# Kernel tuning notes

Hardware: AMD Instinct MI355X
Metric: run time of the kernel (lower is better)

Reference implementation:

```python
import jax, jax.numpy as jnp
import numpy as np

B, CIN, COUT, L = 16, 128, 128, 4096  # kernel_size == L required by the broadcast in the source
STRIDE, DIL, PAD = 1, 1, 0


def setup_inputs() -> dict:
    key = jax.random.key(0)
    kx, kw, kb = jax.random.split(key, 3)
    x = jax.random.normal(kx, (B, CIN, L), dtype=jnp.float32)
    # source does weight.data.int() then .float() in forward -> integer-truncated randn
    weight = jnp.trunc(jax.random.normal(kw, (COUT, CIN, L), dtype=jnp.float32))
    bias = jax.random.normal(kb, (COUT,), dtype=jnp.float32)
    return {"x": x, "weight": weight, "bias": bias}


def reference(x, weight, bias):
    # padding=0 -> F.pad is a no-op; output_size = (L + 2*0 - 1*(K-1) - 1)//1 + 1 = 1
    out_size = (L + 2 * PAD - DIL * (L - 1) - 1) // STRIDE + 1  # == 1
    x_f = jnp.fft.fft(x, axis=2)            # [B, Cin, L] complex64
    w_f = jnp.fft.fft(weight, axis=2)       # [Cout, Cin, L] complex64
    # faithful math of (x_f[:,None] * w_f[None]).sum(dim=2), expressed as a
    # per-frequency complex contraction to avoid the O(B*Cout*Cin*L) intermediate
    out_f = jnp.einsum('bil,oil->bol', x_f, w_f)  # [B, Cout, L]
    out = jnp.fft.ifft(out_f, axis=2).real
    out = out + bias[None, :, None]
    return out[:, :, :out_size]
```

## Files before the change

kernel.cpp:

```cpp
#include <hip/hip_runtime.h>


constexpr int LEN   = 4096;
constexpr int CIN_  = 128;
constexpr int COUT_ = 128;
constexpr int BATCH = 16;

__global__ void init_out_kernel(const float* __restrict__ bias, float* __restrict__ out) {
    int t = blockIdx.x * 256 + threadIdx.x;
    if (t < BATCH * COUT_) out[t] = bias[t & (COUT_ - 1)];
}

__device__ __forceinline__ void gload_lds4(const float* g, float* l) {
    __builtin_amdgcn_global_load_lds(
        (const __attribute__((address_space(1))) unsigned int*)g,
        (__attribute__((address_space(3))) unsigned int*)l, 4, 0, 0);
}

__device__ __forceinline__ void stage_chunk(const float* __restrict__ x, float* dst_base,
                                            int ci, int m0, int wv, int lane) {
#pragma unroll
    for (int bb = 0; bb < 2; ++bb) {
        const int b = 2 * wv + bb;
        const float* xc = x + ((b * CIN_ + ci) << 12);
        float* dstb = dst_base + (b << 9);
#pragma unroll
        for (int t = 0; t < 8; ++t) {
            const int n = (LEN - m0 - (t << 6) - lane) & (LEN - 1);
            gload_lds4(xc + n, dstb + (t << 6));
        }
    }
}

__global__ __launch_bounds__(512, 2)
void conv_fft_dot_kernel(const float* __restrict__ x, const float* __restrict__ w,
                         float* __restrict__ out) {
    __shared__ float lds[17408];

    const int tid   = threadIdx.x;
    const int lane  = tid & 63;
    const int wv    = __builtin_amdgcn_readfirstlane(tid >> 6);
    const int bk    = blockIdx.x;
    const int ot    = bk >> 7;
    const int ci    = bk & 127;
    const int obase = ot * 16 + wv * 2;

    const float* wr0 = w + (((obase + 0) * CIN_ + ci) << 12);
    const float* wr1 = w + (((obase + 1) * CIN_ + ci) << 12);

    float acc[16][2];
#pragma unroll
    for (int b = 0; b < 16; ++b) { acc[b][0] = 0.f; acc[b][1] = 0.f; }

    stage_chunk(x, lds, ci, 0, wv, lane);
    __builtin_amdgcn_sched_barrier(0);
    float4 wa0 = ((const float4*)wr0)[lane];
    float4 wa1 = ((const float4*)wr1)[lane];
    asm volatile("s_waitcnt vmcnt(2)" ::: "memory");
    __builtin_amdgcn_s_barrier();
    __builtin_amdgcn_sched_barrier(0);

#pragma unroll 1
    for (int q = 0; q < 8; ++q) {
        const int m0 = q << 9;
        const float4* __restrict__ xb = (const float4*)(lds + ((q & 1) << 13));

        float4 wb0 = ((const float4*)(wr0 + m0 + 256))[lane];
        float4 wb1 = ((const float4*)(wr1 + m0 + 256))[lane];

        if (q < 7)
            stage_chunk(x, lds + (((q + 1) & 1) << 13), ci, (q + 1) << 9, wv, lane);

#pragma unroll
        for (int b = 0; b < 16; ++b) {
            const float4 xv = xb[(b << 7) + lane];
            acc[b][0] += xv.x * wa0.x; acc[b][0] += xv.y * wa0.y;
            acc[b][0] += xv.z * wa0.z; acc[b][0] += xv.w * wa0.w;
            acc[b][1] += xv.x * wa1.x; acc[b][1] += xv.y * wa1.y;
            acc[b][1] += xv.z * wa1.z; acc[b][1] += xv.w * wa1.w;
        }

        __builtin_amdgcn_sched_barrier(0);

        if (q < 7) {
            wa0 = ((const float4*)(wr0 + m0 + 512))[lane];
            wa1 = ((const float4*)(wr1 + m0 + 512))[lane];
        }

#pragma unroll
        for (int b = 0; b < 16; ++b) {
            const float4 xv = xb[(b << 7) + 64 + lane];
            acc[b][0] += xv.x * wb0.x; acc[b][0] += xv.y * wb0.y;
            acc[b][0] += xv.z * wb0.z; acc[b][0] += xv.w * wb0.w;
            acc[b][1] += xv.x * wb1.x; acc[b][1] += xv.y * wb1.y;
            acc[b][1] += xv.z * wb1.z; acc[b][1] += xv.w * wb1.w;
        }

        if (q < 7) {
            asm volatile("s_waitcnt vmcnt(2)" ::: "memory");
            __builtin_amdgcn_s_barrier();
            __builtin_amdgcn_sched_barrier(0);
        }
    }

    __syncthreads();
#pragma unroll
    for (int b = 0; b < 16; ++b) {
        lds[(wv * 32 + b * 2 + 0) * 68 + lane] = acc[b][0];
        lds[(wv * 32 + b * 2 + 1) * 68 + lane] = acc[b][1];
    }
    __syncthreads();
    if (tid < 256) {
        const float4* row = (const float4*)(lds + tid * 68);
        float sum = 0.f;
#pragma unroll
        for (int l = 0; l < 16; ++l) {
            const float4 v = row[l];
            sum += v.x + v.y + v.z + v.w;
        }
        const int wv2 = tid >> 5, r = tid & 31;
        const int b = r >> 1, jj = r & 1;
        const int o = ot * 16 + wv2 * 2 + jj;
        atomicAdd(out + b * COUT_ + o, sum);
    }
}

extern "C" void kernel_launch(void* const* d_in, const int* in_sizes, int n_in,
                              void* d_out, int out_size, void* d_ws, size_t ws_size,
                              hipStream_t stream) {
    const float* x    = (const float*)d_in[0];
    const float* wgt  = (const float*)d_in[1];
    const float* bias = (const float*)d_in[2];
    float* out = (float*)d_out;
    (void)in_sizes; (void)n_in; (void)d_ws; (void)ws_size; (void)out_size;

    init_out_kernel<<<8, 256, 0, stream>>>(bias, out);
    conv_fft_dot_kernel<<<1024, 512, 0, stream>>>(x, wgt, out);
}
```

Baseline: 393.6 us.

## Widen per-wave output tile to four channels and deepen x staging pipeline

Each wave now computes four output channels instead of two, so every LDS-staged x value is reused twice as often and the grid shrinks to 512 blocks, halving the total number of x reloads. Staging switches to 256-element chunks in a four-deep LDS ring with two chunks in flight, and weights are read with nontemporal loads to avoid polluting cache. The cost is double the accumulator registers (64 floats), which may push occupancy down, plus a four-pass epilogue reduction with extra barriers.

```diff
diff --git a/kernel.cpp b/kernel.cpp
--- a/kernel.cpp
+++ b/kernel.cpp
@@ -6,9 +6,15 @@
 constexpr int COUT_ = 128;
 constexpr int BATCH = 16;
 
+typedef float f32x4 __attribute__((ext_vector_type(4)));
+
 __global__ void init_out_kernel(const float* __restrict__ bias, float* __restrict__ out) {
     int t = blockIdx.x * 256 + threadIdx.x;
     if (t < BATCH * COUT_) out[t] = bias[t & (COUT_ - 1)];
+}
+
+__device__ __forceinline__ f32x4 ntload4(const float* p) {
+    return __builtin_nontemporal_load((const f32x4*)p);
 }
 
 __device__ __forceinline__ void gload_lds4(const float* g, float* l) {
@@ -17,25 +23,22 @@
         (__attribute__((address_space(3))) unsigned int*)l, 4, 0, 0);
 }
 
-__device__ __forceinline__ void stage_chunk(const float* __restrict__ x, float* dst_base,
-                                            int ci, int m0, int wv, int lane) {
+__device__ __forceinline__ void stage256(const float* xc0, const float* xc1,
+                                         float* buf, int m0, int wv, int lane) {
+    float* d0 = buf + ((2 * wv + 0) << 8);
+    float* d1 = buf + ((2 * wv + 1) << 8);
 #pragma unroll
-    for (int bb = 0; bb < 2; ++bb) {
-        const int b = 2 * wv + bb;
-        const float* xc = x + ((b * CIN_ + ci) << 12);
-        float* dstb = dst_base + (b << 9);
-#pragma unroll
-        for (int t = 0; t < 8; ++t) {
-            const int n = (LEN - m0 - (t << 6) - lane) & (LEN - 1);
-            gload_lds4(xc + n, dstb + (t << 6));
-        }
+    for (int t = 0; t < 4; ++t) {
+        const int n = (LEN - m0 - (t << 6) - lane) & (LEN - 1);
+        gload_lds4(xc0 + n, d0 + (t << 6));
+        gload_lds4(xc1 + n, d1 + (t << 6));
     }
 }
 
 __global__ __launch_bounds__(512, 2)
 void conv_fft_dot_kernel(const float* __restrict__ x, const float* __restrict__ w,
                          float* __restrict__ out) {
-    __shared__ float lds[17408];
+    __shared__ float lds[16384];
 
     const int tid   = threadIdx.x;
     const int lane  = tid & 63;
@@ -43,85 +46,101 @@
     const int bk    = blockIdx.x;
     const int ot    = bk >> 7;
     const int ci    = bk & 127;
-    const int obase = ot * 16 + wv * 2;
+    const int obase = ot * 32 + wv * 4;
 
+    const float* xc0 = x + (((2 * wv + 0) * CIN_ + ci) << 12);
+    const float* xc1 = x + (((2 * wv + 1) * CIN_ + ci) << 12);
     const float* wr0 = w + (((obase + 0) * CIN_ + ci) << 12);
     const float* wr1 = w + (((obase + 1) * CIN_ + ci) << 12);
+    const float* wr2 = w + (((obase + 2) * CIN_ + ci) << 12);
+    const float* wr3 = w + (((obase + 3) * CIN_ + ci) << 12);
+    const int lo = lane << 2;
 
-    float acc[16][2];
+    float acc[16][4];
 #pragma unroll
-    for (int b = 0; b < 16; ++b) { acc[b][0] = 0.f; acc[b][1] = 0.f; }
+    for (int b = 0; b < 16; ++b)
+#pragma unroll
+        for (int j = 0; j < 4; ++j) acc[b][j] = 0.f;
 
-    stage_chunk(x, lds, ci, 0, wv, lane);
+    stage256(xc0, xc1, lds, 0, wv, lane);
     __builtin_amdgcn_sched_barrier(0);
-    float4 wa0 = ((const float4*)wr0)[lane];
-    float4 wa1 = ((const float4*)wr1)[lane];
-    asm volatile("s_waitcnt vmcnt(2)" ::: "memory");
+    stage256(xc0, xc1, lds + 4096, 256, wv, lane);
+    __builtin_amdgcn_sched_barrier(0);
+    f32x4 wc[4];
+    wc[0] = ntload4(wr0 + lo); wc[1] = ntload4(wr1 + lo);
+    wc[2] = ntload4(wr2 + lo); wc[3] = ntload4(wr3 + lo);
+    asm volatile("s_waitcnt vmcnt(12)" ::: "memory");
     __builtin_amdgcn_s_barrier();
     __builtin_amdgcn_sched_barrier(0);
 
 #pragma unroll 1
-    for (int q = 0; q < 8; ++q) {
-        const int m0 = q << 9;
-        const float4* __restrict__ xb = (const float4*)(lds + ((q & 1) << 13));
-
-        float4 wb0 = ((const float4*)(wr0 + m0 + 256))[lane];
-        float4 wb1 = ((const float4*)(wr1 + m0 + 256))[lane];
-
-        if (q < 7)
-            stage_chunk(x, lds + (((q + 1) & 1) << 13), ci, (q + 1) << 9, wv, lane);
-
-#pragma unroll
-        for (int b = 0; b < 16; ++b) {
-            const float4 xv = xb[(b << 7) + lane];
-            acc[b][0] += xv.x * wa0.x; acc[b][0] += xv.y * wa0.y;
-            acc[b][0] += xv.z * wa0.z; acc[b][0] += xv.w * wa0.w;
-            acc[b][1] += xv.x * wa1.x; acc[b][1] += xv.y * wa1.y;
-            acc[b][1] += xv.z * wa1.z; acc[b][1] += xv.w * wa1.w;
+    for (int qq = 0; qq < 16; qq += 4) {
+#define BODY(K)                                                               \
+        {                                                                     \
+            const int q  = qq + (K);                                          \
+            const int m0 = q << 8;                                            \
+            f32x4 wn[4];                                                      \
+            if (q < 15) {     \
+                wn[0] = ntload4(wr0 + m0 + 256 + lo);                         \
+                wn[1] = ntload4(wr1 + m0 + 256 + lo);                         \
+                wn[2] = ntload4(wr2 + m0 + 256 + lo);                         \
+                wn[3] = ntload4(wr3 + m0 + 256 + lo);                         \
+            }                                                                 \
+            if (q < 14)       \
+                stage256(xc0, xc1, lds + ((((K) + 2) & 3) << 12),             \
+                         m0 + 512, wv, lane);                                 \
+            __builtin_amdgcn_sched_barrier(0);                                \
+            const float4* xb = (const float4*)(lds + (((K) & 3) << 12));      \
+            _Pragma("unroll")                                                 \
+            for (int b = 0; b < 16; ++b) {                                    \
+                const float4 xv = xb[(b << 6) + lane];                        \
+                _Pragma("unroll")                                             \
+                for (int j = 0; j < 4; ++j) {                                 \
+                    acc[b][j] += xv.x * wc[j].x;                              \
+                    acc[b][j] += xv.y * wc[j].y;                              \
+                    acc[b][j] += xv.z * wc[j].z;                              \
+                    acc[b][j] += xv.w * wc[j].w;                              \
+                }                                                             \
+            }                                                                 \
+            __builtin_amdgcn_sched_barrier(0);                                \
+            if (q < 15) {                                                     \
+                wc[0] = wn[0]; wc[1] = wn[1]; wc[2] = wn[2]; wc[3] = wn[3];   \
+            }                                                                 \
+            if (q < 14)                                                       \
+                asm volatile("s_waitcnt vmcnt(12)" ::: "memory");             \
+            else if (q == 14)                                                 \
+                asm volatile("s_waitcnt vmcnt(4)" ::: "memory");              \
+            if (q < 15) {                                                     \
+                __builtin_amdgcn_s_barrier();                                 \
+                __builtin_amdgcn_sched_barrier(0);                            \
+            }                                                                 \
         }
-
-        __builtin_amdgcn_sched_barrier(0);
-
-        if (q < 7) {
-            wa0 = ((const float4*)(wr0 + m0 + 512))[lane];
-            wa1 = ((const float4*)(wr1 + m0 + 512))[lane];
-        }
-
-#pragma unroll
-        for (int b = 0; b < 16; ++b) {
-            const float4 xv = xb[(b << 7) + 64 + lane];
-            acc[b][0] += xv.x * wb0.x; acc[b][0] += xv.y * wb0.y;
-            acc[b][0] += xv.z * wb0.z; acc[b][0] += xv.w * wb0.w;
-            acc[b][1] += xv.x * wb1.x; acc[b][1] += xv.y * wb1.y;
-            acc[b][1] += xv.z * wb1.z; acc[b][1] += xv.w * wb1.w;
-        }
-
-        if (q < 7) {
-            asm volatile("s_waitcnt vmcnt(2)" ::: "memory");
-            __builtin_amdgcn_s_barrier();
-            __builtin_amdgcn_sched_barrier(0);
-        }
+        BODY(0) BODY(1) BODY(2) BODY(3)
+#undef BODY
     }
 
     __syncthreads();
 #pragma unroll
-    for (int b = 0; b < 16; ++b) {
-        lds[(wv * 32 + b * 2 + 0) * 68 + lane] = acc[b][0];
-        lds[(wv * 32 + b * 2 + 1) * 68 + lane] = acc[b][1];
-    }
-    __syncthreads();
-    if (tid < 256) {
-        const float4* row = (const float4*)(lds + tid * 68);
-        float sum = 0.f;
+    for (int p = 0; p < 4; ++p) {
+        if (p) __syncthreads();
 #pragma unroll
-        for (int l = 0; l < 16; ++l) {
-            const float4 v = row[l];
-            sum += v.x + v.y + v.z + v.w;
+        for (int bb = 0; bb < 4; ++bb)
+#pragma unroll
+            for (int j = 0; j < 4; ++j)
+                lds[(wv * 16 + bb * 4 + j) * 68 + lane] = acc[p * 4 + bb][j];
+        __syncthreads();
+        if (tid < 128) {
+            const float4* row = (const float4*)(lds + tid * 68);
+            float sum = 0.f;
+#pragma unroll
+            for (int l = 0; l < 16; ++l) {
+                const float4 v = row[l];
+                sum += v.x + v.y + v.z + v.w;
+            }
+            const int o = ot * 32 + (tid >> 4) * 4 + (tid & 3);
+            const int b = p * 4 + ((tid >> 2) & 3);
+            atomicAdd(out + b * COUT_ + o, sum);
         }
-        const int wv2 = tid >> 5, r = tid & 31;
-        const int b = r >> 1, jj = r & 1;
-        const int o = ot * 16 + wv2 * 2 + jj;
-        atomicAdd(out + b * COUT_ + o, sum);
     }
 }
 
@@ -135,5 +154,5 @@
     (void)in_sizes; (void)n_in; (void)d_ws; (void)ws_size; (void)out_size;
 
     init_out_kernel<<<8, 256, 0, stream>>>(bias, out);
-    conv_fft_dot_kernel<<<1024, 512, 0, stream>>>(x, wgt, out);
+    conv_fft_dot_kernel<<<512, 512, 0, stream>>>(x, wgt, out);
 }
```

Result: slower. 640.3 us (+62.7%).

## Widen per-wave output tile to four channels, halve block size and LDS

Applied to the files above, without the earlier changes.

Each wave now computes four output channels instead of two, so every x value read from LDS feeds four weight rows, cutting LDS reads per FMA. Blocks shrink to 256 threads with an 8K-float double buffer staged in 256-element chunks, and weights are fetched with nontemporal loads so the streamed weight tensor does not pollute cache. The final reduction is split into four passes to fit the smaller LDS. The cost is more accumulator registers (64 per thread) and fewer waves per block, which may lower the ability to hide latency.

```diff
diff --git a/kernel.cpp b/kernel.cpp
--- a/kernel.cpp
+++ b/kernel.cpp
@@ -6,9 +6,15 @@
 constexpr int COUT_ = 128;
 constexpr int BATCH = 16;
 
+typedef float f32x4 __attribute__((ext_vector_type(4)));
+
 __global__ void init_out_kernel(const float* __restrict__ bias, float* __restrict__ out) {
     int t = blockIdx.x * 256 + threadIdx.x;
     if (t < BATCH * COUT_) out[t] = bias[t & (COUT_ - 1)];
+}
+
+__device__ __forceinline__ f32x4 ntload4(const float* p) {
+    return __builtin_nontemporal_load((const f32x4*)p);
 }
 
 __device__ __forceinline__ void gload_lds4(const float* g, float* l) {
@@ -17,25 +23,38 @@
         (__attribute__((address_space(3))) unsigned int*)l, 4, 0, 0);
 }
 
-__device__ __forceinline__ void stage_chunk(const float* __restrict__ x, float* dst_base,
-                                            int ci, int m0, int wv, int lane) {
-#pragma unroll
-    for (int bb = 0; bb < 2; ++bb) {
-        const int b = 2 * wv + bb;
-        const float* xc = x + ((b * CIN_ + ci) << 12);
-        float* dstb = dst_base + (b << 9);
-#pragma unroll
-        for (int t = 0; t < 8; ++t) {
-            const int n = (LEN - m0 - (t << 6) - lane) & (LEN - 1);
-            gload_lds4(xc + n, dstb + (t << 6));
-        }
+#define STAGE(BUF, M0)                                                     \
+    {                                                                      \
+        _Pragma("unroll")                                                  \
+        for (int t = 0; t < 4; ++t) {                                      \
+            const int n = (LEN - (M0) - (t << 6) - lane) & (LEN - 1);      \
+            gload_lds4(xc0 + n, (BUF) + ((4 * wv + 0) << 8) + (t << 6));   \
+            gload_lds4(xc1 + n, (BUF) + ((4 * wv + 1) << 8) + (t << 6));   \
+            gload_lds4(xc2 + n, (BUF) + ((4 * wv + 2) << 8) + (t << 6));   \
+            gload_lds4(xc3 + n, (BUF) + ((4 * wv + 3) << 8) + (t << 6));   \
+        }                                                                  \
     }
-}
 
-__global__ __launch_bounds__(512, 2)
+#define COMPUTE(BUF, WC)                                                   \
+    {                                                                      \
+        const float4* xb = (const float4*)(BUF);                           \
+        _Pragma("unroll")                                                  \
+        for (int b = 0; b < 16; ++b) {                                     \
+            const float4 xv = xb[(b << 6) + lane];                         \
+            _Pragma("unroll")                                              \
+            for (int j = 0; j < 4; ++j) {                                  \
+                acc[b][j] += xv.x * WC[j].x;                               \
+                acc[b][j] += xv.y * WC[j].y;                               \
+                acc[b][j] += xv.z * WC[j].z;                               \
+                acc[b][j] += xv.w * WC[j].w;                               \
+            }                                                              \
+        }                                                                  \
+    }
+
+__global__ __launch_bounds__(256, 2)
 void conv_fft_dot_kernel(const float* __restrict__ x, const float* __restrict__ w,
                          float* __restrict__ out) {
-    __shared__ float lds[17408];
+    __shared__ float lds[8192];
 
     const int tid   = threadIdx.x;
     const int lane  = tid & 63;
@@ -43,85 +62,93 @@
     const int bk    = blockIdx.x;
     const int ot    = bk >> 7;
     const int ci    = bk & 127;
-    const int obase = ot * 16 + wv * 2;
+    const int obase = ot * 16 + wv * 4;
 
+    const float* xc0 = x + (((4 * wv + 0) * CIN_ + ci) << 12);
+    const float* xc1 = x + (((4 * wv + 1) * CIN_ + ci) << 12);
+    const float* xc2 = x + (((4 * wv + 2) * CIN_ + ci) << 12);
+    const float* xc3 = x + (((4 * wv + 3) * CIN_ + ci) << 12);
     const float* wr0 = w + (((obase + 0) * CIN_ + ci) << 12);
     const float* wr1 = w + (((obase + 1) * CIN_ + ci) << 12);
+    const float* wr2 = w + (((obase + 2) * CIN_ + ci) << 12);
+    const float* wr3 = w + (((obase + 3) * CIN_ + ci) << 12);
+    const int lo = lane << 2;
 
-    float acc[16][2];
+    float acc[16][4];
 #pragma unroll
-    for (int b = 0; b < 16; ++b) { acc[b][0] = 0.f; acc[b][1] = 0.f; }
+    for (int b = 0; b < 16; ++b)
+#pragma unroll
+        for (int j = 0; j < 4; ++j) acc[b][j] = 0.f;
 
-    stage_chunk(x, lds, ci, 0, wv, lane);
+    f32x4 wcA[4], wcB[4];
+
+    STAGE(lds, 0)
     __builtin_amdgcn_sched_barrier(0);
-    float4 wa0 = ((const float4*)wr0)[lane];
-    float4 wa1 = ((const float4*)wr1)[lane];
-    asm volatile("s_waitcnt vmcnt(2)" ::: "memory");
+    wcA[0] = ntload4(wr0 + lo); wcA[1] = ntload4(wr1 + lo);
+    wcA[2] = ntload4(wr2 + lo); wcA[3] = ntload4(wr3 + lo);
+    asm volatile("s_waitcnt vmcnt(4)" ::: "memory");
     __builtin_amdgcn_s_barrier();
     __builtin_amdgcn_sched_barrier(0);
 
 #pragma unroll 1
-    for (int q = 0; q < 8; ++q) {
-        const int m0 = q << 9;
-        const float4* __restrict__ xb = (const float4*)(lds + ((q & 1) << 13));
-
-        float4 wb0 = ((const float4*)(wr0 + m0 + 256))[lane];
-        float4 wb1 = ((const float4*)(wr1 + m0 + 256))[lane];
-
-        if (q < 7)
-            stage_chunk(x, lds + (((q + 1) & 1) << 13), ci, (q + 1) << 9, wv, lane);
-
-#pragma unroll
-        for (int b = 0; b < 16; ++b) {
-            const float4 xv = xb[(b << 7) + lane];
-            acc[b][0] += xv.x * wa0.x; acc[b][0] += xv.y * wa0.y;
-            acc[b][0] += xv.z * wa0.z; acc[b][0] += xv.w * wa0.w;
-            acc[b][1] += xv.x * wa1.x; acc[b][1] += xv.y * wa1.y;
-            acc[b][1] += xv.z * wa1.z; acc[b][1] += xv.w * wa1.w;
-        }
-
-        __builtin_amdgcn_sched_barrier(0);
-
-        if (q < 7) {
-            wa0 = ((const float4*)(wr0 + m0 + 512))[lane];
-            wa1 = ((const float4*)(wr1 + m0 + 512))[lane];
-        }
-
-#pragma unroll
-        for (int b = 0; b < 16; ++b) {
-            const float4 xv = xb[(b << 7) + 64 + lane];
-            acc[b][0] += xv.x * wb0.x; acc[b][0] += xv.y * wb0.y;
-            acc[b][0] += xv.z * wb0.z; acc[b][0] += xv.w * wb0.w;
-            acc[b][1] += xv.x * wb1.x; acc[b][1] += xv.y * wb1.y;
-            acc[b][1] += xv.z * wb1.z; acc[b][1] += xv.w * wb1.w;
-        }
-
-        if (q < 7) {
-            asm volatile("s_waitcnt vmcnt(2)" ::: "memory");
+    for (int qq = 0; qq < 16; qq += 2) {
+        {
+            const int m0 = qq << 8;
+            STAGE(lds + 4096, m0 + 256)
+            __builtin_amdgcn_sched_barrier(0);
+            wcB[0] = ntload4(wr0 + m0 + 256 + lo);
+            wcB[1] = ntload4(wr1 + m0 + 256 + lo);
+            wcB[2] = ntload4(wr2 + m0 + 256 + lo);
+            wcB[3] = ntload4(wr3 + m0 + 256 + lo);
+            __builtin_amdgcn_sched_barrier(0);
+            COMPUTE(lds, wcA)
+            asm volatile("s_waitcnt vmcnt(4)" ::: "memory");
             __builtin_amdgcn_s_barrier();
             __builtin_amdgcn_sched_barrier(0);
+        }
+        {
+            const int q  = qq + 1;
+            const int m0 = q << 8;
+            if (q < 15) {
+                STAGE(lds, m0 + 256)
+                __builtin_amdgcn_sched_barrier(0);
+                wcA[0] = ntload4(wr0 + m0 + 256 + lo);
+                wcA[1] = ntload4(wr1 + m0 + 256 + lo);
+                wcA[2] = ntload4(wr2 + m0 + 256 + lo);
+                wcA[3] = ntload4(wr3 + m0 + 256 + lo);
+            }
+            __builtin_amdgcn_sched_barrier(0);
+            COMPUTE(lds + 4096, wcB)
+            if (q < 15) {
+                asm volatile("s_waitcnt vmcnt(4)" ::: "memory");
+                __builtin_amdgcn_s_barrier();
+                __builtin_amdgcn_sched_barrier(0);
+            }
         }
     }
 
     __syncthreads();
 #pragma unroll
-    for (int b = 0; b < 16; ++b) {
-        lds[(wv * 32 + b * 2 + 0) * 68 + lane] = acc[b][0];
-        lds[(wv * 32 + b * 2 + 1) * 68 + lane] = acc[b][1];
-    }
-    __syncthreads();
-    if (tid < 256) {
-        const float4* row = (const float4*)(lds + tid * 68);
-        float sum = 0.f;
+    for (int p = 0; p < 4; ++p) {
+        if (p) __syncthreads();
 #pragma unroll
-        for (int l = 0; l < 16; ++l) {
-            const float4 v = row[l];
-            sum += v.x + v.y + v.z + v.w;
+        for (int bb = 0; bb < 4; ++bb)
+#pragma unroll
+            for (int j = 0; j < 4; ++j)
+                lds[(wv * 16 + bb * 4 + j) * 68 + lane] = acc[p * 4 + bb][j];
+        __syncthreads();
+        if (tid < 64) {
+            const float4* row = (const float4*)(lds + tid * 68);
+            float sum = 0.f;
+#pragma unroll
+            for (int l = 0; l < 16; ++l) {
+                const float4 v = row[l];
+                sum += v.x + v.y + v.z + v.w;
+            }
+            const int o = ot * 16 + (tid >> 4) * 4 + (tid & 3);
+            const int b = p * 4 + ((tid >> 2) & 3);
+            atomicAdd(out + b * COUT_ + o, sum);
         }
-        const int wv2 = tid >> 5, r = tid & 31;
-        const int b = r >> 1, jj = r & 1;
-        const int o = ot * 16 + wv2 * 2 + jj;
-        atomicAdd(out + b * COUT_ + o, sum);
     }
 }
 
@@ -135,5 +162,5 @@
     (void)in_sizes; (void)n_in; (void)d_ws; (void)ws_size; (void)out_size;
 
     init_out_kernel<<<8, 256, 0, stream>>>(bias, out);
-    conv_fft_dot_kernel<<<1024, 512, 0, stream>>>(x, wgt, out);
+    conv_fft_dot_kernel<<<1024, 256, 0, stream>>>(x, wgt, out);
 }
```

Result: faster. 372.4 us, median of 2 (-5.4%).
